# Kernel optimization log

Measured on AMD Instinct MI355X. Metric: run time of the kernel, lower is better.

Reference implementation:

```python
import jax, jax.numpy as jnp
import numpy as np

LN_EPS = 1e-5

def _layer_norm(x):
    mu = jnp.mean(x, axis=-1, keepdims=True)
    var = jnp.var(x, axis=-1, keepdims=True)
    return (x - mu) / jnp.sqrt(var + LN_EPS)


def setup_inputs() -> dict:
    key = jax.random.key(0)
    ks = jax.random.split(key, 3)
    B, C, H, W = 8, 384, 48, 48
    x = jax.random.normal(ks[0], (B, C, H, W), dtype=jnp.float32)
    # torch Linear default init ~ U(-1/sqrt(fan_in), 1/sqrt(fan_in)); scaled normal is fine for a reference
    W1 = jax.random.normal(ks[1], (3 * C, C), dtype=jnp.float32) / np.sqrt(C)
    b1 = jnp.zeros((3 * C,), dtype=jnp.float32)
    W2 = jax.random.normal(ks[2], (C, C), dtype=jnp.float32) / np.sqrt(C)
    b2 = jnp.zeros((C,), dtype=jnp.float32)
    return {"x": x, "W1": W1, "b1": b1, "W2": W2, "b2": b2}


def reference(x, W1, b1, W2, b2):
    num_heads = 6
    B, C, H, W = x.shape
    N = H * W
    d = C // num_heads
    # [B,C,H,W] -> [B,N,C]
    t = x.reshape(B, C, N).transpose(0, 2, 1)
    t_norm = _layer_norm(t)
    qkv = t_norm @ W1.T + b1                      # [B,N,3C]
    q, k, v = jnp.split(qkv, 3, axis=-1)
    q = q.reshape(B, N, num_heads, d).transpose(0, 2, 1, 3)  # [B,h,N,d]
    k = k.reshape(B, N, num_heads, d).transpose(0, 2, 1, 3)
    v = v.reshape(B, N, num_heads, d).transpose(0, 2, 1, 3)
    att = jnp.einsum('bhnd,bhmd->bhnm', q, k) / jnp.sqrt(jnp.float32(d))
    att = jax.nn.softmax(att, axis=-1)            # dropout_prob = 0.0 -> identity
    o = jnp.einsum('bhnm,bhmd->bhnd', att, v)     # [B,h,N,d]
    o = o.transpose(0, 2, 1, 3).reshape(B, N, C)
    o = o @ W2.T + b2
    out = (o + t_norm).transpose(0, 2, 1).reshape(B, C, H, W)
    return out
```

## Files before the change

### kernel.cpp

```cpp
#include <hip/hip_runtime.h>
#include <cstdint>

#define DEVI __device__ __forceinline__

typedef unsigned short u16;
typedef __attribute__((ext_vector_type(4))) u16 u16x4;
typedef __attribute__((ext_vector_type(2))) unsigned int u32x2;
typedef __attribute__((ext_vector_type(2))) float f32x2;
typedef __attribute__((ext_vector_type(4))) float f32x4;
typedef __attribute__((ext_vector_type(8))) float f32x8;
typedef __attribute__((ext_vector_type(16))) float f32x16;
typedef __attribute__((ext_vector_type(8))) __bf16 bf16x8;

constexpr int kB = 8, kC = 384, kN = 2304, kNH = 6, kD = 64;
constexpr int kM = kB * kN;
constexpr int k3C = 3 * kC;
constexpr int kNT = kN / 64;
constexpr int kKS = kC / 32;
constexpr int kW1E = k3C * kC;
constexpr int kW2E = kC * kC;

DEVI float bf2f(u16 u) {
  union { unsigned int u; float f; } v; v.u = ((unsigned int)u) << 16; return v.f;
}
DEVI u16 f2bf(float f) {
  union { float f; unsigned int u; } v; v.f = f;
  return (u16)((v.u + 0x7fffu + ((v.u >> 16) & 1u)) >> 16);
}
DEVI void gload16(const void* g, void* l) {
  __builtin_amdgcn_global_load_lds(
      (__attribute__((address_space(1))) void*)const_cast<void*>(g),
      (__attribute__((address_space(3))) void*)l, 16, 0, 0);
}
DEVI bf16x8 ldg8(const u16* p) { return *reinterpret_cast<const bf16x8*>(p); }

DEVI float fexp2(float x) {
#if __has_builtin(__builtin_amdgcn_exp2f)
  return __builtin_amdgcn_exp2f(x);
#else
  return exp2f(x);
#endif
}

DEVI unsigned cvtpk(float lo, float hi) {
  unsigned r;
  asm("v_cvt_pk_bf16_f32 %0, %1, %2" : "=v"(r) : "v"(lo), "v"(hi));
  return r;
}
DEVI void plswap(unsigned& a, unsigned& b) {
#if __has_builtin(__builtin_amdgcn_permlane32_swap)
  auto rr = __builtin_amdgcn_permlane32_swap(a, b, false, false);
  a = rr[0]; b = rr[1];
#else
  unsigned ax = __shfl_xor(a, 32, 64), bx = __shfl_xor(b, 32, 64);
  int hi = (threadIdx.x & 63) >> 5;
  unsigned r0 = hi ? bx : a;
  unsigned r1 = hi ? b : ax;
  a = r0; b = r1;
#endif
}

DEVI bf16x8 ldsw(const u16* base, int row, int cb) {
  return *reinterpret_cast<const bf16x8*>(
      (const char*)base + row * 128 + (cb ^ ((row & 7) << 4)));
}

__global__ __launch_bounds__(256) void ln_cast_kernel(const float* __restrict__ x,
                                                      u16* __restrict__ tn,
                                                      const float* __restrict__ W1,
                                                      const float* __restrict__ W2,
                                                      u16* __restrict__ w1b,
                                                      u16* __restrict__ w2b) {
  if (blockIdx.x >= 288) {
    const int gid = (blockIdx.x - 288) * 256 + threadIdx.x;
    const int i4 = gid * 4;
    if (i4 < kW1E) {
      f32x4 v = *reinterpret_cast<const f32x4*>(&W1[i4]);
      u16x4 o;
#pragma unroll
      for (int r = 0; r < 4; ++r) o[r] = f2bf(v[r]);
      *reinterpret_cast<u16x4*>(&w1b[i4]) = o;
    } else if (i4 < kW1E + kW2E) {
      const int j = i4 - kW1E;
      f32x4 v = *reinterpret_cast<const f32x4*>(&W2[j]);
      u16x4 o;
#pragma unroll
      for (int r = 0; r < 4; ++r) o[r] = f2bf(v[r]);
      *reinterpret_cast<u16x4*>(&w2b[j]) = o;
    }
    return;
  }
  const int b = blockIdx.x & 7;
  const int n0 = (blockIdx.x >> 3) * 64;
  const int t = threadIdx.x;
  const int tni = t & 63, tc = t >> 6;
  const float* xb = x + (size_t)b * kC * kN;

  float sum = 0.f, ssq = 0.f;
  for (int c = tc; c < kC; c += 4) {
    float v = xb[(size_t)c * kN + n0 + tni];
    sum += v; ssq += v * v;
  }
  __shared__ float red[8][64];
  red[tc][tni] = sum; red[tc + 4][tni] = ssq;
  __syncthreads();
  __shared__ float s_mu[64], s_rs[64];
  if (t < 64) {
    float s = red[0][t] + red[1][t] + red[2][t] + red[3][t];
    float q = red[4][t] + red[5][t] + red[6][t] + red[7][t];
    float mu = s * (1.f / kC);
    float var = q * (1.f / kC) - mu * mu;
    s_mu[t] = mu; s_rs[t] = rsqrtf(var + 1e-5f);
  }
  __syncthreads();
  __shared__ float tile[64][65];
  for (int c0 = 0; c0 < kC; c0 += 64) {
#pragma unroll
    for (int kk = 0; kk < 16; ++kk) {
      int cl = tc * 16 + kk;
      tile[tni][cl] = xb[(size_t)(c0 + cl) * kN + n0 + tni];
    }
    __syncthreads();
#pragma unroll
    for (int kk = 0; kk < 16; ++kk) {
      int nl = tc * 16 + kk;
      float v = (tile[nl][tni] - s_mu[nl]) * s_rs[nl];
      tn[((size_t)b * kN + n0 + nl) * kC + c0 + tni] = f2bf(v);
    }
    __syncthreads();
  }
}

DEVI int swzg(int r, int sl) { return (sl ^ ((r >> 1) & 3)) * 8; }

#define GSTAGE(dstLds, gbase, kt)                                        \
  {                                                                      \
    _Pragma("unroll")                                                    \
    for (int c = 0; c < 2; ++c) {                                        \
      int i = c * 256 + t;                                               \
      int r = i >> 2, sl = i & 3;                                        \
      gload16((gbase) + (size_t)r * kC + (kt) + swzg(r, sl),             \
              (dstLds) + (c * 256 + (t & 192)) * 8);                     \
    }                                                                    \
  }

DEVI void gemm_core(const u16* __restrict__ A, const u16* __restrict__ Bm,
                    f32x4 acc[4][4], u16* lA, u16* lB) {
  const int t = threadIdx.x;
  const int lane = t & 63;
  const int w = t >> 6, wr = w >> 1, wc = w & 1;
  const int lr = lane & 15, lg = lane >> 4;

  GSTAGE(lA, A, 0)
  GSTAGE(lB, Bm, 0)

  int cur = 0;
#pragma unroll 3
  for (int s = 0; s < kKS; ++s) {
    const u16* cA = lA + cur * 4096;
    const u16* cB = lB + cur * 4096;
    const int nxt = (cur == 2) ? 0 : cur + 1;
    if (s + 1 < kKS) {
      GSTAGE(lA + nxt * 4096, A, (s + 1) * 32)
      GSTAGE(lB + nxt * 4096, Bm, (s + 1) * 32)
      asm volatile("s_waitcnt vmcnt(4)" ::: "memory");
    } else {
      asm volatile("s_waitcnt vmcnt(0)" ::: "memory");
    }
    __builtin_amdgcn_s_barrier();
    __builtin_amdgcn_sched_barrier(0);

    bf16x8 af[4], bfr[4];
#pragma unroll
    for (int f = 0; f < 4; ++f) {
      int row = wr * 64 + f * 16 + lr;
      af[f] = ldg8(&cA[row * 32 + swzg(row, lg)]);
    }
#pragma unroll
    for (int f = 0; f < 4; ++f) {
      int row = wc * 64 + f * 16 + lr;
      bfr[f] = ldg8(&cB[row * 32 + swzg(row, lg)]);
    }
    __builtin_amdgcn_s_setprio(1);
#pragma unroll
    for (int fm = 0; fm < 4; ++fm)
#pragma unroll
      for (int fn = 0; fn < 4; ++fn)
        acc[fm][fn] = __builtin_amdgcn_mfma_f32_16x16x32_bf16(af[fm], bfr[fn], acc[fm][fn], 0, 0, 0);
    __builtin_amdgcn_s_setprio(0);
    cur = nxt;
  }
}

#define GSTAGE2A(dstLds, gbase, kt)                                      \
  {                                                                      \
    _Pragma("unroll")                                                    \
    for (int c = 0; c < 2; ++c) {                                        \
      int i = c * 512 + t;                                               \
      int r = i >> 2, sl = i & 3;                                        \
      gload16((gbase) + (size_t)r * kC + (kt) + swzg(r, sl),             \
              (dstLds) + (c * 512 + (t & 448)) * 8);                     \
    }                                                                    \
  }
#define GSTAGE2B(dstLds, gbase, kt)                                      \
  {                                                                      \
    int r = t >> 2, sl = t & 3;                                          \
    gload16((gbase) + (size_t)r * kC + (kt) + swzg(r, sl),               \
            (dstLds) + (t & 448) * 8);                                   \
  }

DEVI void gemm_core256(const u16* __restrict__ A, const u16* __restrict__ Bm,
                       f32x4 acc[4][4], u16* lA, u16* lB) {
  const int t = threadIdx.x;
  const int lane = t & 63;
  const int w = t >> 6, wr = w >> 1, wc = w & 1;
  const int lr = lane & 15, lg = lane >> 4;

  GSTAGE2A(lA, A, 0)
  GSTAGE2B(lB, Bm, 0)

  int cur = 0;
#pragma unroll 3
  for (int s = 0; s < kKS; ++s) {
    const u16* cA = lA + cur * 8192;
    const u16* cB = lB + cur * 4096;
    const int nxt = (cur == 2) ? 0 : cur + 1;
    if (s + 1 < kKS) {
      GSTAGE2A(lA + nxt * 8192, A, (s + 1) * 32)
      GSTAGE2B(lB + nxt * 4096, Bm, (s + 1) * 32)
      asm volatile("s_waitcnt vmcnt(3)" ::: "memory");
    } else {
      asm volatile("s_waitcnt vmcnt(0)" ::: "memory");
    }
    __builtin_amdgcn_s_barrier();
    __builtin_amdgcn_sched_barrier(0);

    bf16x8 af[4], bfr[4];
#pragma unroll
    for (int f = 0; f < 4; ++f) {
      int row = wr * 64 + f * 16 + lr;
      af[f] = ldg8(&cA[row * 32 + swzg(row, lg)]);
    }
#pragma unroll
    for (int f = 0; f < 4; ++f) {
      int row = wc * 64 + f * 16 + lr;
      bfr[f] = ldg8(&cB[row * 32 + swzg(row, lg)]);
    }
    __builtin_amdgcn_s_setprio(1);
#pragma unroll
    for (int fm = 0; fm < 4; ++fm)
#pragma unroll
      for (int fn = 0; fn < 4; ++fn)
        acc[fm][fn] = __builtin_amdgcn_mfma_f32_16x16x32_bf16(af[fm], bfr[fn], acc[fm][fn], 0, 0, 0);
    __builtin_amdgcn_s_setprio(0);
    cur = nxt;
  }
}

__global__ __launch_bounds__(512) void qkv_kernel(const u16* __restrict__ tn, const u16* __restrict__ w1b,
                                                  const float* __restrict__ b1,
                                                  u16* __restrict__ q, u16* __restrict__ kbuf,
                                                  u16* __restrict__ vTout) {
  __shared__ u16 shmem[36864];
  const int wg = blockIdx.x;
  const int xcd = wg & 7, idx = wg >> 3;
  const int m0 = (xcd * 9 + idx / 9) * 256;
  const int o0 = (idx % 9) * 128;
  f32x4 acc[4][4] = {};
  gemm_core256(tn + (size_t)m0 * kC, w1b + (size_t)o0 * kC, acc, shmem, shmem + 3 * 8192);

  const int t = threadIdx.x, lane = t & 63, w = t >> 6;
  const int wr = w >> 1, wc = w & 1, lr = lane & 15, lg = lane >> 4;
  const float kQScale = 0.125f * 1.44269504088896f;
  const int bb = xcd;
  const int nb0 = (idx / 9) * 256;
  const int ot = o0 >> 7;

  if (ot >= 6) {
#pragma unroll
    for (int fn = 0; fn < 4; ++fn) {
      int ol = o0 - 2 * kC + wc * 64 + fn * 16 + lr;
      float bias = b1[2 * kC + ol];
      int h = ol >> 6, dd = ol & 63;
#pragma unroll
      for (int fm = 0; fm < 4; ++fm) {
        int n4 = nb0 + wr * 64 + fm * 16 + lg * 4;
        u16x4 pk;
#pragma unroll
        for (int r = 0; r < 4; ++r) pk[r] = f2bf(acc[fm][fn][r] + bias);
        *reinterpret_cast<u16x4*>(&vTout[(((size_t)bb * kNH + h) * kD + dd) * kN + n4]) = pk;
      }
    }
  } else {
    __syncthreads();
    const float scale = (ot < 3) ? kQScale : 1.0f;
#pragma unroll
    for (int fn = 0; fn < 4; ++fn) {
      int col = wc * 64 + fn * 16 + lr;
      float bias = b1[o0 + col];
#pragma unroll
      for (int fm = 0; fm < 4; ++fm)
#pragma unroll
        for (int r = 0; r < 4; ++r) {
          int row = wr * 64 + fm * 16 + lg * 4 + r;
          shmem[row * 132 + col] = f2bf((acc[fm][fn][r] + bias) * scale);
        }
    }
    __syncthreads();
    u16* outp = (ot < 3) ? q : kbuf;
    const int h0 = (o0 - (ot < 3 ? 0 : kC)) >> 6;
#pragma unroll
    for (int it = 0; it < 8; ++it) {
      int ci = it * 512 + t;
      int row = ci >> 4, ck = ci & 15;
      int c = ck * 8;
      int h = h0 + (c >> 6), dd = c & 63;
      *reinterpret_cast<bf16x8*>(&outp[(((size_t)bb * kNH + h) * kN + nb0 + row) * kD + dd]) =
          *reinterpret_cast<const bf16x8*>(&shmem[row * 132 + c]);
    }
  }
}

#define PV_STEP(SV, OFF, KS)                                                          \
  {                                                                                   \
    unsigned a0 = cvtpk(SV[OFF + 0], SV[OFF + 1]);                                    \
    unsigned a1 = cvtpk(SV[OFF + 2], SV[OFF + 3]);                                    \
    unsigned a2 = cvtpk(SV[OFF + 4], SV[OFF + 5]);                                    \
    unsigned a3 = cvtpk(SV[OFF + 6], SV[OFF + 7]);                                    \
    plswap(a0, a2); plswap(a1, a3);                                                   \
    union { unsigned wds[4]; bf16x8 v; } pu;                                          \
    pu.wds[0] = a0; pu.wds[1] = a1; pu.wds[2] = a2; pu.wds[3] = a3;                   \
    bf16x8 vf0 = ldsw(vL, ql, (KS) * 32 + hi * 16);                                   \
    bf16x8 vf1 = ldsw(vL, 32 + ql, (KS) * 32 + hi * 16);                              \
    o0 = __builtin_amdgcn_mfma_f32_32x32x16_bf16(vf0, pu.v, o0, 0, 0, 0);             \
    o1 = __builtin_amdgcn_mfma_f32_32x32x16_bf16(vf1, pu.v, o1, 0, 0, 0);             \
    o2 = __builtin_amdgcn_mfma_f32_32x32x16_bf16(onesf, pu.v, o2, 0, 0, 0);           \
  }

#define STAGE(dstLds, gbase, gstride)                                                 \
  {                                                                                   \
    int r_ = t >> 3;                                                                  \
    int cb_ = ((t & 7) * 16) ^ ((r_ & 7) << 4);                                       \
    gload16((gbase) + (size_t)r_ * (gstride) + cb_,                                   \
            (dstLds) + (t & 448) * 8);                                                \
  }

__global__ __launch_bounds__(512) void attn_kernel(const u16* __restrict__ qg, const u16* __restrict__ kg,
                                                   const u16* __restrict__ vT, u16* __restrict__ obuf) {
  const int wg = blockIdx.x;
  const int xcd = wg & 7, idx = wg >> 3;
  const int bh = xcd * 6 + idx / 9;
  const int qt = idx % 9;
  const int b = bh / kNH, h = bh % kNH;
  const int t = threadIdx.x, lane = t & 63, w = t >> 6;
  const int q0w = qt * 256 + w * 32;
  const int ql = lane & 31;
  const int hi = lane >> 5;
  const u16* qb  = qg + (size_t)bh * kN * kD;
  const char* kbB = (const char*)(kg + (size_t)bh * kN * kD);
  const char* vbT = (const char*)(vT + (size_t)bh * kD * kN);

  __shared__ u16 kLds[4 * 4096];
  __shared__ u16 vLds[4 * 4096];

  bf16x8 qf[4];
#pragma unroll
  for (int ds = 0; ds < 4; ++ds)
    qf[ds] = ldg8(&qb[(size_t)(q0w + ql) * kD + ds * 16 + hi * 8]);

  bf16x8 onesf;
#pragma unroll
  for (int j = 0; j < 8; ++j) onesf[j] = (__bf16)1.0f;

  f32x16 o0 = {}, o1 = {}, o2 = {};

  STAGE(kLds, kbB, 128)
  STAGE(vLds, vbT, kN * 2)
  STAGE(kLds + 4096, kbB + (size_t)64 * 128, 128)
  STAGE(vLds + 4096, vbT + 128, kN * 2)

  int cur = 0;
  for (int ti = 0; ti < kNT; ++ti) {
    const u16* kL = kLds + cur * 4096;
    const u16* vL = vLds + cur * 4096;
    if (ti + 2 < kNT) {
      const int stg = (cur + 2) & 3;
      const char* kNext = kbB + (size_t)(ti + 2) * 64 * 128;
      const char* vNext = vbT + (size_t)(ti + 2) * 128;
      STAGE(kLds + stg * 4096, kNext, 128)
      STAGE(vLds + stg * 4096, vNext, kN * 2)
      asm volatile("s_waitcnt vmcnt(4)" ::: "memory");
    } else if (ti + 1 < kNT) {
      asm volatile("s_waitcnt vmcnt(2)" ::: "memory");
    } else {
      asm volatile("s_waitcnt vmcnt(0)" ::: "memory");
    }
    __builtin_amdgcn_s_barrier();
    __builtin_amdgcn_sched_barrier(0);

    f32x16 s0 = {}, s1 = {};
#pragma unroll
    for (int ds = 0; ds < 4; ++ds) {
      bf16x8 kf0 = ldsw(kL, ql, ds * 32 + hi * 16);
      bf16x8 kf1 = ldsw(kL, 32 + ql, ds * 32 + hi * 16);
      s0 = __builtin_amdgcn_mfma_f32_32x32x16_bf16(kf0, qf[ds], s0, 0, 0, 0);
      s1 = __builtin_amdgcn_mfma_f32_32x32x16_bf16(kf1, qf[ds], s1, 0, 0, 0);
    }

#pragma unroll
    for (int r = 0; r < 16; ++r) {
      s0[r] = fexp2(s0[r]);
      s1[r] = fexp2(s1[r]);
    }

    PV_STEP(s0, 0, 0)
    PV_STEP(s0, 8, 1)
    PV_STEP(s1, 0, 2)
    PV_STEP(s1, 8, 3)

    cur = (cur + 1) & 3;
  }

  const float inv = 1.f / o2[0];
  {
    const size_t row = ((size_t)b * kN + q0w + ql) * kC + h * 64;
#pragma unroll
    for (int g = 0; g < 4; ++g) {
      u32x2 pk;
      pk.x = cvtpk(o0[g * 4 + 0] * inv, o0[g * 4 + 1] * inv);
      pk.y = cvtpk(o0[g * 4 + 2] * inv, o0[g * 4 + 3] * inv);
      *reinterpret_cast<u32x2*>(&obuf[row + g * 8 + 4 * hi]) = pk;
    }
#pragma unroll
    for (int g = 0; g < 4; ++g) {
      u32x2 pk;
      pk.x = cvtpk(o1[g * 4 + 0] * inv, o1[g * 4 + 1] * inv);
      pk.y = cvtpk(o1[g * 4 + 2] * inv, o1[g * 4 + 3] * inv);
      *reinterpret_cast<u32x2*>(&obuf[row + 32 + g * 8 + 4 * hi]) = pk;
    }
  }
}

__global__ __launch_bounds__(256) void proj_kernel(const u16* __restrict__ obuf, const u16* __restrict__ w2b,
                                                   const float* __restrict__ b2, const u16* __restrict__ tn,
                                                   float* __restrict__ out) {
  __shared__ u16 lAs[3 * 4096], lBs[3 * 4096];
  const int wg = blockIdx.x;
  const int xcd = wg & 7, idx = wg >> 3;
  const int bn = xcd * 18 + idx / 3;
  const int b = bn / 18;
  const int n0 = (bn % 18) * 128;
  const int c0 = (idx % 3) * 128;
  f32x4 acc[4][4] = {};
  gemm_core(w2b + (size_t)c0 * kC, obuf + ((size_t)b * kN + n0) * kC, acc, lAs, lBs);

  const int t = threadIdx.x, lane = t & 63, w = t >> 6;
  const int wr = w >> 1, wc = w & 1, lr = lane & 15, lg = lane >> 4;
#pragma unroll
  for (int fm = 0; fm < 4; ++fm)
#pragma unroll
    for (int fn = 0; fn < 4; ++fn) {
      int n = n0 + wc * 64 + fn * 16 + lr;
#pragma unroll
      for (int r = 0; r < 4; ++r) {
        int c = c0 + wr * 64 + fm * 16 + lg * 4 + r;
        float val = acc[fm][fn][r] + b2[c] + bf2f(tn[((size_t)b * kN + n) * kC + c]);
        out[((size_t)b * kC + c) * kN + n] = val;
      }
    }
}

extern "C" void kernel_launch(void* const* d_in, const int* in_sizes, int n_in,
                              void* d_out, int out_size, void* d_ws, size_t ws_size,
                              hipStream_t stream) {
  const float* x  = (const float*)d_in[0];
  const float* W1 = (const float*)d_in[1];
  const float* b1 = (const float*)d_in[2];
  const float* W2 = (const float*)d_in[3];
  const float* b2 = (const float*)d_in[4];
  float* out = (float*)d_out;

  const size_t nBNC = (size_t)kM * kC;
  u16* tn  = (u16*)d_ws;
  u16* qb  = tn  + nBNC;
  u16* kb  = qb  + nBNC;
  u16* vb  = kb  + nBNC;
  u16* vT  = vb  + nBNC;
  u16* w1b = vT  + nBNC;
  u16* w2b = w1b + (size_t)k3C * kC;
  u16* obuf = vb;

  ln_cast_kernel<<<dim3(288 + 576), dim3(256), 0, stream>>>(x, tn, W1, W2, w1b, w2b);
  qkv_kernel<<<dim3(8 * 81), dim3(512), 0, stream>>>(tn, w1b, b1, qb, kb, vT);
  attn_kernel<<<dim3((kN / 256) * kB * kNH), dim3(512), 0, stream>>>(qb, kb, vT, obuf);
  proj_kernel<<<dim3((kN / 128) * (kC / 128) * kB), dim3(256), 0, stream>>>(obuf, w2b, b2, tn, out);
}
```

Before: 165.5 us.

## Process two query tiles per wave in attention and sum softmax denominators on VALU

The attention kernel now runs 4 waves of 256 threads, and each wave covers 64 query rows (two 32-row sub-tiles) instead of 32. Each K and V fragment read from LDS is therefore reused across two sets of MFMAs, which halves LDS reads per unit of work. The row-sum MFMA against a ones matrix is dropped; the sums are accumulated with vector adds and reduced at the end with a cross-lane shuffle. Staging is adjusted so that fewer threads issue two loads each, and the waitcnt values are doubled to match. The costs are much higher register pressure from twice as many accumulators and fewer waves per block, which can hurt latency hiding.

```diff
diff --git a/kernel.cpp b/kernel.cpp
--- a/kernel.cpp
+++ b/kernel.cpp
@@ -321,31 +321,43 @@
   }
 }
 
-#define PV_STEP(SV, OFF, KS)                                                          \
+#define PV_STEP2(SVa, SVb, OFF, KS)                                                   \
   {                                                                                   \
-    unsigned a0 = cvtpk(SV[OFF + 0], SV[OFF + 1]);                                    \
-    unsigned a1 = cvtpk(SV[OFF + 2], SV[OFF + 3]);                                    \
-    unsigned a2 = cvtpk(SV[OFF + 4], SV[OFF + 5]);                                    \
-    unsigned a3 = cvtpk(SV[OFF + 6], SV[OFF + 7]);                                    \
-    plswap(a0, a2); plswap(a1, a3);                                                   \
-    union { unsigned wds[4]; bf16x8 v; } pu;                                          \
-    pu.wds[0] = a0; pu.wds[1] = a1; pu.wds[2] = a2; pu.wds[3] = a3;                   \
     bf16x8 vf0 = ldsw(vL, ql, (KS) * 32 + hi * 16);                                   \
     bf16x8 vf1 = ldsw(vL, 32 + ql, (KS) * 32 + hi * 16);                              \
-    o0 = __builtin_amdgcn_mfma_f32_32x32x16_bf16(vf0, pu.v, o0, 0, 0, 0);             \
-    o1 = __builtin_amdgcn_mfma_f32_32x32x16_bf16(vf1, pu.v, o1, 0, 0, 0);             \
-    o2 = __builtin_amdgcn_mfma_f32_32x32x16_bf16(onesf, pu.v, o2, 0, 0, 0);           \
+    unsigned a0 = cvtpk(SVa[OFF + 0], SVa[OFF + 1]);                                  \
+    unsigned a1 = cvtpk(SVa[OFF + 2], SVa[OFF + 3]);                                  \
+    unsigned a2 = cvtpk(SVa[OFF + 4], SVa[OFF + 5]);                                  \
+    unsigned a3 = cvtpk(SVa[OFF + 6], SVa[OFF + 7]);                                  \
+    plswap(a0, a2); plswap(a1, a3);                                                   \
+    union { unsigned wds[4]; bf16x8 v; } puA;                                         \
+    puA.wds[0] = a0; puA.wds[1] = a1; puA.wds[2] = a2; puA.wds[3] = a3;               \
+    o0a = __builtin_amdgcn_mfma_f32_32x32x16_bf16(vf0, puA.v, o0a, 0, 0, 0);          \
+    o1a = __builtin_amdgcn_mfma_f32_32x32x16_bf16(vf1, puA.v, o1a, 0, 0, 0);          \
+    unsigned b0 = cvtpk(SVb[OFF + 0], SVb[OFF + 1]);                                  \
+    unsigned b1_ = cvtpk(SVb[OFF + 2], SVb[OFF + 3]);                                 \
+    unsigned b2_ = cvtpk(SVb[OFF + 4], SVb[OFF + 5]);                                 \
+    unsigned b3 = cvtpk(SVb[OFF + 6], SVb[OFF + 7]);                                  \
+    plswap(b0, b2_); plswap(b1_, b3);                                                 \
+    union { unsigned wds[4]; bf16x8 v; } puB;                                         \
+    puB.wds[0] = b0; puB.wds[1] = b1_; puB.wds[2] = b2_; puB.wds[3] = b3;             \
+    o0b = __builtin_amdgcn_mfma_f32_32x32x16_bf16(vf0, puB.v, o0b, 0, 0, 0);          \
+    o1b = __builtin_amdgcn_mfma_f32_32x32x16_bf16(vf1, puB.v, o1b, 0, 0, 0);          \
   }
 
 #define STAGE(dstLds, gbase, gstride)                                                 \
   {                                                                                   \
-    int r_ = t >> 3;                                                                  \
-    int cb_ = ((t & 7) * 16) ^ ((r_ & 7) << 4);                                       \
-    gload16((gbase) + (size_t)r_ * (gstride) + cb_,                                   \
-            (dstLds) + (t & 448) * 8);                                                \
-  }
-
-__global__ __launch_bounds__(512) void attn_kernel(const u16* __restrict__ qg, const u16* __restrict__ kg,
+    _Pragma("unroll")                                                                 \
+    for (int c = 0; c < 2; ++c) {                                                     \
+      int i = c * 256 + t;                                                            \
+      int r = i >> 3;                                                                 \
+      int cb = ((i & 7) * 16) ^ ((r & 7) << 4);                                       \
+      gload16((gbase) + (size_t)r * (gstride) + cb,                                   \
+              (dstLds) + c * 2048 + (t & 192) * 8);                                   \
+    }                                                                                 \
+  }
+
+__global__ __launch_bounds__(256) void attn_kernel(const u16* __restrict__ qg, const u16* __restrict__ kg,
                                                    const u16* __restrict__ vT, u16* __restrict__ obuf) {
   const int wg = blockIdx.x;
   const int xcd = wg & 7, idx = wg >> 3;
@@ -353,7 +365,7 @@
   const int qt = idx % 9;
   const int b = bh / kNH, h = bh % kNH;
   const int t = threadIdx.x, lane = t & 63, w = t >> 6;
-  const int q0w = qt * 256 + w * 32;
+  const int q0w = qt * 256 + w * 64;
   const int ql = lane & 31;
   const int hi = lane >> 5;
   const u16* qb  = qg + (size_t)bh * kN * kD;
@@ -363,16 +375,15 @@
   __shared__ u16 kLds[4 * 4096];
   __shared__ u16 vLds[4 * 4096];
 
-  bf16x8 qf[4];
-#pragma unroll
-  for (int ds = 0; ds < 4; ++ds)
-    qf[ds] = ldg8(&qb[(size_t)(q0w + ql) * kD + ds * 16 + hi * 8]);
-
-  bf16x8 onesf;
-#pragma unroll
-  for (int j = 0; j < 8; ++j) onesf[j] = (__bf16)1.0f;
-
-  f32x16 o0 = {}, o1 = {}, o2 = {};
+  bf16x8 qfa[4], qfb[4];
+#pragma unroll
+  for (int ds = 0; ds < 4; ++ds) {
+    qfa[ds] = ldg8(&qb[(size_t)(q0w + ql) * kD + ds * 16 + hi * 8]);
+    qfb[ds] = ldg8(&qb[(size_t)(q0w + 32 + ql) * kD + ds * 16 + hi * 8]);
+  }
+
+  f32x16 o0a = {}, o1a = {}, o0b = {}, o1b = {};
+  f32x16 lsumA = {}, lsumB = {};
 
   STAGE(kLds, kbB, 128)
   STAGE(vLds, vbT, kN * 2)
@@ -385,58 +396,95 @@
     const u16* vL = vLds + cur * 4096;
     if (ti + 2 < kNT) {
       const int stg = (cur + 2) & 3;
-      const char* kNext = kbB + (size_t)(ti + 2) * 64 * 128;
-      const char* vNext = vbT + (size_t)(ti + 2) * 128;
-      STAGE(kLds + stg * 4096, kNext, 128)
-      STAGE(vLds + stg * 4096, vNext, kN * 2)
+      STAGE(kLds + stg * 4096, kbB + (size_t)(ti + 2) * 64 * 128, 128)
+      STAGE(vLds + stg * 4096, vbT + (size_t)(ti + 2) * 128, kN * 2)
+      asm volatile("s_waitcnt vmcnt(8)" ::: "memory");
+    } else if (ti + 1 < kNT) {
       asm volatile("s_waitcnt vmcnt(4)" ::: "memory");
-    } else if (ti + 1 < kNT) {
-      asm volatile("s_waitcnt vmcnt(2)" ::: "memory");
     } else {
       asm volatile("s_waitcnt vmcnt(0)" ::: "memory");
     }
     __builtin_amdgcn_s_barrier();
     __builtin_amdgcn_sched_barrier(0);
 
-    f32x16 s0 = {}, s1 = {};
+    f32x16 s0a = {}, s1a = {}, s0b = {}, s1b = {};
 #pragma unroll
     for (int ds = 0; ds < 4; ++ds) {
       bf16x8 kf0 = ldsw(kL, ql, ds * 32 + hi * 16);
       bf16x8 kf1 = ldsw(kL, 32 + ql, ds * 32 + hi * 16);
-      s0 = __builtin_amdgcn_mfma_f32_32x32x16_bf16(kf0, qf[ds], s0, 0, 0, 0);
-      s1 = __builtin_amdgcn_mfma_f32_32x32x16_bf16(kf1, qf[ds], s1, 0, 0, 0);
+      s0a = __builtin_amdgcn_mfma_f32_32x32x16_bf16(kf0, qfa[ds], s0a, 0, 0, 0);
+      s1a = __builtin_amdgcn_mfma_f32_32x32x16_bf16(kf1, qfa[ds], s1a, 0, 0, 0);
+      s0b = __builtin_amdgcn_mfma_f32_32x32x16_bf16(kf0, qfb[ds], s0b, 0, 0, 0);
+      s1b = __builtin_amdgcn_mfma_f32_32x32x16_bf16(kf1, qfb[ds], s1b, 0, 0, 0);
     }
 
 #pragma unroll
     for (int r = 0; r < 16; ++r) {
-      s0[r] = fexp2(s0[r]);
-      s1[r] = fexp2(s1[r]);
-    }
-
-    PV_STEP(s0, 0, 0)
-    PV_STEP(s0, 8, 1)
-    PV_STEP(s1, 0, 2)
-    PV_STEP(s1, 8, 3)
+      s0a[r] = fexp2(s0a[r]);
+      s1a[r] = fexp2(s1a[r]);
+      s0b[r] = fexp2(s0b[r]);
+      s1b[r] = fexp2(s1b[r]);
+    }
+    lsumA += s0a; lsumA += s1a;
+    lsumB += s0b; lsumB += s1b;
+
+    PV_STEP2(s0a, s0b, 0, 0)
+    PV_STEP2(s0a, s0b, 8, 1)
+    PV_STEP2(s1a, s1b, 0, 2)
+    PV_STEP2(s1a, s1b, 8, 3)
 
     cur = (cur + 1) & 3;
   }
 
-  const float inv = 1.f / o2[0];
+  f32x8 ra8 = __builtin_shufflevector(lsumA, lsumA, 0, 1, 2, 3, 4, 5, 6, 7) +
+              __builtin_shufflevector(lsumA, lsumA, 8, 9, 10, 11, 12, 13, 14, 15);
+  f32x4 ra4 = __builtin_shufflevector(ra8, ra8, 0, 1, 2, 3) +
+              __builtin_shufflevector(ra8, ra8, 4, 5, 6, 7);
+  f32x2 ra2 = __builtin_shufflevector(ra4, ra4, 0, 1) +
+              __builtin_shufflevector(ra4, ra4, 2, 3);
+  float la = ra2.x + ra2.y;
+  la += __shfl_xor(la, 32, 64);
+  f32x8 rb8 = __builtin_shufflevector(lsumB, lsumB, 0, 1, 2, 3, 4, 5, 6, 7) +
+              __builtin_shufflevector(lsumB, lsumB, 8, 9, 10, 11, 12, 13, 14, 15);
+  f32x4 rb4 = __builtin_shufflevector(rb8, rb8, 0, 1, 2, 3) +
+              __builtin_shufflevector(rb8, rb8, 4, 5, 6, 7);
+  f32x2 rb2 = __builtin_shufflevector(rb4, rb4, 0, 1) +
+              __builtin_shufflevector(rb4, rb4, 2, 3);
+  float lb = rb2.x + rb2.y;
+  lb += __shfl_xor(lb, 32, 64);
+
+  const float inva = 1.f / la;
+  const float invb = 1.f / lb;
   {
-    const size_t row = ((size_t)b * kN + q0w + ql) * kC + h * 64;
+    const size_t rowA = ((size_t)b * kN + q0w + ql) * kC + h * 64;
+    const size_t rowB = ((size_t)b * kN + q0w + 32 + ql) * kC + h * 64;
 #pragma unroll
     for (int g = 0; g < 4; ++g) {
       u32x2 pk;
-      pk.x = cvtpk(o0[g * 4 + 0] * inv, o0[g * 4 + 1] * inv);
-      pk.y = cvtpk(o0[g * 4 + 2] * inv, o0[g * 4 + 3] * inv);
-      *reinterpret_cast<u32x2*>(&obuf[row + g * 8 + 4 * hi]) = pk;
+      pk.x = cvtpk(o0a[g * 4 + 0] * inva, o0a[g * 4 + 1] * inva);
+      pk.y = cvtpk(o0a[g * 4 + 2] * inva, o0a[g * 4 + 3] * inva);
+      *reinterpret_cast<u32x2*>(&obuf[rowA + g * 8 + 4 * hi]) = pk;
     }
 #pragma unroll
     for (int g = 0; g < 4; ++g) {
       u32x2 pk;
-      pk.x = cvtpk(o1[g * 4 + 0] * inv, o1[g * 4 + 1] * inv);
-      pk.y = cvtpk(o1[g * 4 + 2] * inv, o1[g * 4 + 3] * inv);
-      *reinterpret_cast<u32x2*>(&obuf[row + 32 + g * 8 + 4 * hi]) = pk;
+      pk.x = cvtpk(o1a[g * 4 + 0] * inva, o1a[g * 4 + 1] * inva);
+      pk.y = cvtpk(o1a[g * 4 + 2] * inva, o1a[g * 4 + 3] * inva);
+      *reinterpret_cast<u32x2*>(&obuf[rowA + 32 + g * 8 + 4 * hi]) = pk;
+    }
+#pragma unroll
+    for (int g = 0; g < 4; ++g) {
+      u32x2 pk;
+      pk.x = cvtpk(o0b[g * 4 + 0] * invb, o0b[g * 4 + 1] * invb);
+      pk.y = cvtpk(o0b[g * 4 + 2] * invb, o0b[g * 4 + 3] * invb);
+      *reinterpret_cast<u32x2*>(&obuf[rowB + g * 8 + 4 * hi]) = pk;
+    }
+#pragma unroll
+    for (int g = 0; g < 4; ++g) {
+      u32x2 pk;
+      pk.x = cvtpk(o1b[g * 4 + 0] * invb, o1b[g * 4 + 1] * invb);
+      pk.y = cvtpk(o1b[g * 4 + 2] * invb, o1b[g * 4 + 3] * invb);
+      *reinterpret_cast<u32x2*>(&obuf[rowB + 32 + g * 8 + 4 * hi]) = pk;
     }
   }
 }
@@ -492,6 +540,6 @@
 
   ln_cast_kernel<<<dim3(288 + 576), dim3(256), 0, stream>>>(x, tn, W1, W2, w1b, w2b);
   qkv_kernel<<<dim3(8 * 81), dim3(512), 0, stream>>>(tn, w1b, b1, qb, kb, vT);
-  attn_kernel<<<dim3((kN / 256) * kB * kNH), dim3(512), 0, stream>>>(qb, kb, vT, obuf);
+  attn_kernel<<<dim3((kN / 256) * kB * kNH), dim3(256), 0, stream>>>(qb, kb, vT, obuf);
   proj_kernel<<<dim3((kN / 128) * (kC / 128) * kB), dim3(256), 0, stream>>>(obuf, w2b, b2, tn, out);
 }
```

Result: slower. 187.6 us (+13.3%).
